# Performance work log

Hardware: AMD Instinct MI355X
Metric: run time of the kernel (lower is better)

The kernel has to match this reference:

```python
import jax, jax.numpy as jnp
import numpy as np
from jax import lax

NUM_TAGS = 64
PAD = 0


def setup_inputs() -> dict:
    key = jax.random.key(0)
    k1, k2, k3 = jax.random.split(key, 3)
    B, S, T = 128, 512, NUM_TAGS
    features = jax.random.normal(k1, (B, S, T), dtype=jnp.float32)
    labels = jax.random.randint(k2, (B, S), 0, T, dtype=jnp.int64)
    mask = jnp.ones((B, S), dtype=jnp.float32)
    transitions = jax.random.normal(k3, (T, T), dtype=jnp.float32)
    transitions = transitions.at[PAD, :].set(-10000.0)
    transitions = transitions.at[:, PAD].set(-10000.0)
    return {"features": features, "labels": labels, "mask": mask,
            "transitions": transitions}


def _score_sequence(emissions, labels, mask, transitions):
    # emission score at the gold labels, masked
    em = jnp.take_along_axis(emissions, labels[:, :, None], axis=2)[:, :, 0]
    seq_em = jnp.sum(em * mask, axis=1)
    # transition scores between consecutive gold labels
    tr = transitions[labels[:, :-1], labels[:, 1:]]
    tr_mask = mask[:, :-1] * mask[:, 1:]
    seq_tr = jnp.sum(tr * tr_mask, axis=1)
    return seq_em + seq_tr  # (B,)


def _log_partition(emissions, mask, transitions):
    # forward algorithm over the sequence via lax.scan
    alpha0 = emissions[:, 0, :]  # (B, T)
    em_rest = jnp.swapaxes(emissions[:, 1:, :], 0, 1)  # (S-1, B, T)
    mk_rest = jnp.swapaxes(mask[:, 1:], 0, 1)          # (S-1, B)

    def step(alpha, xs):
        em_t, m_t = xs
        # scores[b, i, j] = alpha[b, i] + transitions[i, j] + em_t[b, j]
        scores = alpha[:, :, None] + transitions[None, :, :] + em_t[:, None, :]
        new_alpha = jax.nn.logsumexp(scores, axis=1)  # (B, T)
        m = m_t[:, None]
        new_alpha = new_alpha * m + alpha * (1.0 - m)
        return new_alpha, None

    alpha, _ = lax.scan(step, alpha0, (em_rest, mk_rest))
    return jax.nn.logsumexp(alpha, axis=1)  # (B,)


def reference(features, labels, mask, transitions):
    gold = _score_sequence(features, labels, mask, transitions)
    logZ = _log_partition(features, mask, transitions)
    return jnp.mean(logZ - gold)  # scalar NLL
```

## Files before the change

### kernel.cpp

```cpp
#include <hip/hip_runtime.h>

#define B 128
#define S 512
#define T 64

typedef short bf16x8 __attribute__((ext_vector_type(8)));
typedef float f32x4 __attribute__((ext_vector_type(4)));
typedef _Float16 h2 __attribute__((ext_vector_type(2)));

__device__ __forceinline__ float rdlane(float v, int l) {
    return __int_as_float(__builtin_amdgcn_readlane(__float_as_int(v), l));
}
__device__ __forceinline__ unsigned cvtpk_bf16(float lo, float hi) {
    unsigned r;
    asm("v_cvt_pk_bf16_f32 %0, %1, %2" : "=v"(r) : "v"(lo), "v"(hi));
    return r;
}
__device__ __forceinline__ float fast_exp2(float x) {
    float r;
    asm("v_exp_f32 %0, %1" : "=v"(r) : "v"(x));
    return r;
}
__device__ __forceinline__ f32x4 mfma_init(bf16x8 a, bf16x8 b, f32x4 c0) {
    f32x4 d;
    asm volatile("v_mfma_f32_16x16x32_bf16 %0, %1, %2, %3"
                 : "=&v"(d) : "v"(a), "v"(b), "v"(c0));
    return d;
}
__device__ __forceinline__ void mfma_acc(f32x4& c, bf16x8 a, bf16x8 b) {
    asm volatile("v_mfma_f32_16x16x32_bf16 %0, %1, %2, %0"
                 : "+v"(c) : "v"(a), "v"(b));
}
__device__ __forceinline__ int krow(int kt, int gq, int e) {
    return 32 * kt + ((e >> 2) << 4) + 4 * gq + (e & 3);
}

template<int GG>
__global__ __launch_bounds__(256, 3)
void crf_chunk4(const float* __restrict__ features,
                const float* __restrict__ mask,
                const float* __restrict__ transitions,
                unsigned short* __restrict__ Zout,
                int* __restrict__ Kout)
{
    constexpr int CLT = S / GG;
    __shared__ unsigned short relay[4][T * 68];

    const int wid  = threadIdx.x >> 6;
    const int lane = threadIdx.x & 63;
    const int idx  = blockIdx.x * 4 + wid;
    const int b  = idx / GG;
    const int g  = idx % GG;
    const int c  = lane & 15;
    const int gq = lane >> 4;

    bf16x8 Ef[4][2];
    #pragma unroll
    for (int rt = 0; rt < 4; ++rt)
      #pragma unroll
      for (int kt = 0; kt < 2; ++kt) {
          unsigned dw[4];
          #pragma unroll
          for (int w = 0; w < 4; ++w) {
              int k0 = krow(kt, gq, 2 * w);
              float x0 = __expf(transitions[k0       * T + (c + 16*rt)]);
              float x1 = __expf(transitions[(k0 + 1) * T + (c + 16*rt)]);
              dw[w] = cvtpk_bf16(x0, x1);
          }
          uint4 q; q.x = dw[0]; q.y = dw[1]; q.z = dw[2]; q.w = dw[3];
          Ef[rt][kt] = __builtin_bit_cast(bf16x8, q);
      }

    bf16x8 Bf[2][4];
    #pragma unroll
    for (int kt = 0; kt < 2; ++kt)
      #pragma unroll
      for (int ct = 0; ct < 4; ++ct)
        #pragma unroll
        for (int e = 0; e < 8; ++e)
            Bf[kt][ct][e] = (krow(kt, gq, e) == 16*ct + c) ? (short)0x3F80
                                                           : (short)0;

    const float* fb = features + (size_t)b * S * T;
    const float* mb = mask + (size_t)b * S;
    const int t0 = g * CLT + 1;
    const int t1 = (g == GG - 1) ? S : (t0 + CLT);

    const f32x4 zero4 = {0.f, 0.f, 0.f, 0.f};

    int ktot = 0;
    float zloc = 1.0f;
    float mxr  = 1.0f;

    f32x4 emP[4];
    #pragma unroll
    for (int rt = 0; rt < 4; ++rt)
        emP[rt] = *(const f32x4*)(fb + t0 * T + 16*rt + 4*gq);
    float mP = mb[t0];

    for (int w = 0; w < CLT / 4; ++w) {
        #pragma unroll
        for (int j = 0; j < 4; ++j) {
            const int t = t0 + 4 * w + j;
            const bool act = (t < t1);

            f32x4 emc[4];
            #pragma unroll
            for (int rt = 0; rt < 4; ++rt) emc[rt] = emP[rt];
            float mc = mP;
            {
                int tn = min(t + 1, S - 1);
                #pragma unroll
                for (int rt = 0; rt < 4; ++rt)
                    emP[rt] = *(const f32x4*)(fb + tn * T + 16*rt + 4*gq);
                mP = mb[tn];
            }

            int kc = 0;
            if (j == 0) {
                kc = ((__float_as_int(mxr) >> 23) & 0xFF) - 127;
                kc = kc < -30 ? -30 : (kc > 60 ? 60 : kc);
            }

            if (act && mc != 0.0f) {
                if (j == 0) ktot += kc;
                const float kcf = (j == 0) ? (float)kc : 0.0f;

                f32x4 d4[4];
                #pragma unroll
                for (int rt = 0; rt < 4; ++rt)
                    #pragma unroll
                    for (int r = 0; r < 4; ++r)
                        d4[rt][r] = fast_exp2(fmaf(emc[rt][r], 1.44269504f, -kcf));

                #pragma unroll
                for (int ct = 0; ct < 4; ++ct) {
                    f32x4 Ct[4];
                    #pragma unroll
                    for (int tr = 0; tr < 4; ++tr) {
                        f32x4 z = mfma_init(Ef[tr][0], Bf[0][ct], zero4);
                        mfma_acc(z, Ef[tr][1], Bf[1][ct]);
                        Ct[tr] = z;
                    }
                    asm volatile("s_nop 7\ns_nop 7");
                    #pragma unroll
                    for (int tr = 0; tr < 4; ++tr) {
                        Ct[tr] *= d4[tr];
                        zloc = fmaxf(zloc, fmaxf(fmaxf(Ct[tr][0], Ct[tr][1]),
                                                 fmaxf(Ct[tr][2], Ct[tr][3])));
                    }
                    uint4 q0, q1;
                    q0.x = cvtpk_bf16(Ct[0][0], Ct[0][1]);
                    q0.y = cvtpk_bf16(Ct[0][2], Ct[0][3]);
                    q0.z = cvtpk_bf16(Ct[1][0], Ct[1][1]);
                    q0.w = cvtpk_bf16(Ct[1][2], Ct[1][3]);
                    q1.x = cvtpk_bf16(Ct[2][0], Ct[2][1]);
                    q1.y = cvtpk_bf16(Ct[2][2], Ct[2][3]);
                    q1.z = cvtpk_bf16(Ct[3][0], Ct[3][1]);
                    q1.w = cvtpk_bf16(Ct[3][2], Ct[3][3]);
                    Bf[0][ct] = __builtin_bit_cast(bf16x8, q0);
                    Bf[1][ct] = __builtin_bit_cast(bf16x8, q1);
                }
            }

            if (j == 2) {
                float mr = zloc;
                #pragma unroll
                for (int o = 32; o > 0; o >>= 1)
                    mr = fmaxf(mr, __shfl_xor(mr, o));
                mxr = mr; zloc = 1.0f;
            }
        }
    }

    unsigned short* rl = relay[wid];
    #pragma unroll
    for (int kt = 0; kt < 2; ++kt)
      #pragma unroll
      for (int ct = 0; ct < 4; ++ct) {
          uint4 q = __builtin_bit_cast(uint4, Bf[kt][ct]);
          int col = 16*ct + c;
          uint2 wa; wa.x = q.x; wa.y = q.y;
          uint2 wb; wb.x = q.z; wb.y = q.w;
          *(uint2*)&rl[col * 68 + 32*kt      + 4*gq] = wa;
          *(uint2*)&rl[col * 68 + 32*kt + 16 + 4*gq] = wb;
      }
    asm volatile("s_waitcnt lgkmcnt(0)" ::: "memory");

    unsigned short* zo = Zout + ((size_t)(b * GG + g)) * 64 * 64;
    #pragma unroll
    for (int q8 = 0; q8 < 8; ++q8) {
        unsigned dw[4];
        #pragma unroll
        for (int d = 0; d < 4; ++d) {
            unsigned lo = rl[(8*q8 + 2*d    ) * 68 + lane];
            unsigned hi = rl[(8*q8 + 2*d + 1) * 68 + lane];
            dw[d] = lo | (hi << 16);
        }
        uint4 wv; wv.x = dw[0]; wv.y = dw[1]; wv.z = dw[2]; wv.w = dw[3];
        *(uint4*)(zo + (size_t)lane * 64 + 8*q8) = wv;
    }
    if (lane == 0) Kout[b * GG + g] = ktot;
}

template<int GG>
__global__ __launch_bounds__(64, 1)
void crf_apply(const float* __restrict__ features,
               const int*   __restrict__ labels,
               const float* __restrict__ mask,
               const float* __restrict__ transitions,
               const unsigned short* __restrict__ Zmat,
               const int*   __restrict__ Kscale,
               float*       __restrict__ res)
{
    __shared__ float trans_lds[T * T];
    __shared__ float bcast[2][T];
    const int lane = threadIdx.x;
    const int b = blockIdx.x;

    for (int i = 0; i < T; ++i)
        trans_lds[i * T + lane] = transitions[i * T + lane];
    __syncthreads();

    const float* fb = features + (size_t)b * S * T;
    const int*   lb = labels + (size_t)b * S;
    const float* mb = mask + (size_t)b * S;

    float gold = 0.f;
    #pragma unroll
    for (int ch = 0; ch < S / T; ++ch) {
        int tt = ch * T + lane;
        int tm1 = tt > 0 ? tt - 1 : 0;
        int la = lb[tt], lp = lb[tm1];
        float mt = mb[tt], mp = mb[tm1];
        float em_g = fb[(size_t)tt * T + la];
        float tr_g = trans_lds[lp * T + la];
        gold += em_g * mt + ((tt > 0) ? tr_g * (mp * mt) : 0.f);
    }

    float a0 = fb[lane];
    float A0 = a0;
    #pragma unroll
    for (int o = 32; o > 0; o >>= 1) A0 = fmaxf(A0, __shfl_xor(A0, o));
    float v = __expf(a0 - A0);

    int esum = 0;

    const unsigned short* zb = Zmat + ((size_t)b * GG) * 64 * 64 + (size_t)lane * 64;
    uint4 cur[8], n1[8], n2[8];
    #pragma unroll
    for (int i = 0; i < 8; ++i) cur[i] = ((const uint4*)zb)[i];
    #pragma unroll
    for (int i = 0; i < 8; ++i) n1[i] = ((const uint4*)(zb + 64 * 64))[i];
    #pragma unroll
    for (int i = 0; i < 8; ++i) n2[i] = ((const uint4*)(zb + 2 * 64 * 64))[i];

    for (int g = 0; g < GG; ++g) {
        const int buf = g & 1;
        bcast[buf][lane] = v;
        asm volatile("s_waitcnt lgkmcnt(0)" ::: "memory");
        f32x4 vb[16];
        #pragma unroll
        for (int q = 0; q < 16; ++q) vb[q] = ((const f32x4*)bcast[buf])[q];

        float ac0 = 0.f, ac1 = 0.f, ac2 = 0.f, ac3 = 0.f;
        #pragma unroll
        for (int i = 0; i < 8; ++i) {
            unsigned zz[4] = {cur[i].x, cur[i].y, cur[i].z, cur[i].w};
            #pragma unroll
            for (int d = 0; d < 4; ++d) {
                int k = i * 8 + d * 2;
                float f0 = __int_as_float(zz[d] << 16);
                float f1 = __int_as_float(zz[d] & 0xFFFF0000u);
                if ((d & 1) == 0) { ac0 = fmaf(f0, vb[k >> 2][k & 3], ac0);
                                    ac1 = fmaf(f1, vb[(k+1) >> 2][(k+1) & 3], ac1); }
                else             { ac2 = fmaf(f0, vb[k >> 2][k & 3], ac2);
                                    ac3 = fmaf(f1, vb[(k+1) >> 2][(k+1) & 3], ac3); }
            }
        }
        float acc = (ac0 + ac1) + (ac2 + ac3);

        float a1 = fmaxf(rdlane(acc, 1), 1e-30f);
        int e = ((__float_as_int(a1) >> 23) & 0xFF) - 127;
        v = acc * __int_as_float((unsigned)(127 - e) << 23);
        esum += e + Kscale[b * GG + g];

        #pragma unroll
        for (int i = 0; i < 8; ++i) { cur[i] = n1[i]; n1[i] = n2[i]; }
        if (g + 3 < GG) {
            const uint4* zn = (const uint4*)(zb + (size_t)(g + 3) * 64 * 64);
            #pragma unroll
            for (int i = 0; i < 8; ++i) n2[i] = zn[i];
        }
    }

    float sum = v;
    #pragma unroll
    for (int o = 32; o > 0; o >>= 1) sum += __shfl_xor(sum, o);
    float logZ = __logf(fmaxf(sum, 1e-30f)) + A0 + (float)esum * 0.69314718056f;

    #pragma unroll
    for (int o = 32; o > 0; o >>= 1) gold += __shfl_xor(gold, o);

    if (lane == 0) res[b] = logZ - gold;
}

__global__ __launch_bounds__(64, 1)
void crf_fwd_seq(const float* __restrict__ features,
                 const int*   __restrict__ labels,
                 const float* __restrict__ mask,
                 const float* __restrict__ transitions,
                 float*       __restrict__ ws)
{
    __shared__ float trans_lds[T * T];
    __shared__ __align__(16) _Float16 ea_lds[2][T];

    const int lane = threadIdx.x;
    const int b    = blockIdx.x;

    for (int i = 0; i < T; ++i)
        trans_lds[i * T + lane] = transitions[i * T + lane];
    __syncthreads();

    h2 etr[T / 2];
    #pragma unroll
    for (int k = 0; k < T / 2; ++k) {
        etr[k].x = (_Float16)__expf(trans_lds[(2 * k + 0) * T + lane]);
        etr[k].y = (_Float16)__expf(trans_lds[(2 * k + 1) * T + lane]);
    }

    const float* fb = features + (size_t)b * S * T;
    const float* mb = mask + (size_t)b * S;
    const int*   lb = labels + (size_t)b * S;

    float alpha = fb[lane];
    float gold_part = 0.f;
    float M = 0.f;

    float em_n1 = fb[1 * T + lane];
    float em_n2 = fb[2 * T + lane];
    float em_n3 = fb[3 * T + lane];

    int   lab_c = lb[lane];
    int   lab_p = lb[lane > 0 ? lane - 1 : 0];
    float m_c   = mb[lane];
    float m_p   = mb[lane > 0 ? lane - 1 : 0];

    for (int ch = 0; ch < S / T; ++ch) {
        const int base = ch * T;
        const int tt   = base + lane;

        const int   glab  = lab_c;
        const int   glabp = lab_p;
        const float gmc   = m_c;
        const float gmp   = m_p;
        const float mreg  = m_c;

        float em_g = fb[(size_t)tt * T + glab];
        float tr_g = trans_lds[glabp * T + glab];

        {
            int tn  = tt + T;  if (tn > S - 1) tn = S - 1;
            int tnp = tn - 1;  if (tnp < 0) tnp = 0;
            lab_c = lb[tn]; lab_p = lb[tnp];
            m_c   = mb[tn]; m_p   = mb[tnp];
        }

        const int i0 = (ch == 0) ? 1 : 0;
        #pragma unroll 4
        for (int i = i0; i < T; ++i) {
            const int t = base + i;
            float em = em_n1;
            em_n1 = em_n2; em_n2 = em_n3;
            int tn = t + 3; if (tn > S - 1) tn = S - 1;
            em_n3 = fb[tn * T + lane];

            float ea = __expf(alpha - M);
            ea_lds[t & 1][lane] = (_Float16)ea;
            asm volatile("s_waitcnt lgkmcnt(0)" ::: "memory");

            const uint4* ep = (const uint4*)&ea_lds[t & 1][0];
            float a0 = 0.f, a1 = 0.f, a2 = 0.f, a3 = 0.f;
            #pragma unroll
            for (int q = 0; q < 8; ++q) {
                uint4 r = ep[q];
                a0 = __builtin_amdgcn_fdot2(__builtin_bit_cast(h2, r.x), etr[4 * q + 0], a0, false);
                a1 = __builtin_amdgcn_fdot2(__builtin_bit_cast(h2, r.y), etr[4 * q + 1], a1, false);
                a2 = __builtin_amdgcn_fdot2(__builtin_bit_cast(h2, r.z), etr[4 * q + 2], a2, false);
                a3 = __builtin_amdgcn_fdot2(__builtin_bit_cast(h2, r.w), etr[4 * q + 3], a3, false);
            }
            float s = (a0 + a1) + (a2 + a3);

            float m_t = rdlane(mreg, i);
            float s1  = rdlane(s, 1);
            float em1 = rdlane(em, 1);
            float Mn  = M + __logf(s1) + em1;

            float val = M + __logf(s) + em;
            val = fmaxf(val, -1e30f);
            alpha = val * m_t + alpha * (1.f - m_t);
            M     = (m_t > 0.5f) ? Mn : M;
        }

        float valid = (tt > 0) ? 1.f : 0.f;
        gold_part += em_g * gmc + tr_g * (gmp * gmc) * valid;
    }

    float M2 = alpha;
    #pragma unroll
    for (int o = 32; o > 0; o >>= 1) M2 = fmaxf(M2, __shfl_xor(M2, o));
    float e2 = __expf(alpha - M2);
    #pragma unroll
    for (int o = 32; o > 0; o >>= 1) e2 += __shfl_xor(e2, o);
    float logZ = M2 + __logf(e2);

    #pragma unroll
    for (int o = 32; o > 0; o >>= 1) gold_part += __shfl_xor(gold_part, o);

    if (lane == 0) ws[b] = logZ - gold_part;
}

__global__ __launch_bounds__(128)
void crf_reduce(const float* __restrict__ ws, float* __restrict__ out)
{
    const int tid = threadIdx.x;
    float v = ws[tid];
    #pragma unroll
    for (int o = 32; o > 0; o >>= 1) v += __shfl_xor(v, o);

    __shared__ float partial[2];
    if ((tid & 63) == 0) partial[tid >> 6] = v;
    __syncthreads();
    if (tid == 0) out[0] = (partial[0] + partial[1]) * (1.0f / (float)B);
}

extern "C" void kernel_launch(void* const* d_in, const int* in_sizes, int n_in,
                              void* d_out, int out_size, void* d_ws, size_t ws_size,
                              hipStream_t stream)
{
    const float* features    = (const float*)d_in[0];
    const int*   labels      = (const int*)  d_in[1];
    const float* mask        = (const float*)d_in[2];
    const float* transitions = (const float*)d_in[3];
    float* out = (float*)d_out;

    constexpr int GG = 16;
    const size_t zbytes = (size_t)B * GG * 64 * 64 * sizeof(unsigned short);
    const size_t kbytes = (size_t)B * GG * sizeof(int);
    const size_t need   = zbytes + kbytes + (size_t)B * sizeof(float);

    if (ws_size >= need) {
        unsigned short* Zmat = (unsigned short*)d_ws;
        int*   Ks  = (int*)((char*)d_ws + zbytes);
        float* res = (float*)((char*)d_ws + zbytes + kbytes);
        crf_chunk4<GG><<<dim3(B * GG / 4), dim3(256), 0, stream>>>(features, mask, transitions, Zmat, Ks);
        crf_apply<GG><<<dim3(B), dim3(64), 0, stream>>>(features, labels, mask, transitions, Zmat, Ks, res);
        crf_reduce<<<dim3(1), dim3(128), 0, stream>>>(res, out);
    } else {
        float* res = (float*)d_ws;
        crf_fwd_seq<<<dim3(B), dim3(64), 0, stream>>>(features, labels, mask, transitions, res);
        crf_reduce<<<dim3(1), dim3(128), 0, stream>>>(res, out);
    }
}
```

Before: 69.60 us.

## Split each chunk's 64 columns across four waves with per-column-group scales

The chunk kernel used to give one wave a whole 64x64 chunk product. It now uses one block per (batch, chunk), with each of the four waves carrying 16 columns. Each wave keeps its own exponent scale, so Kscale now stores four values per chunk, and the apply kernel rescales partial dot products by column group. This cuts the serial MFMA chain per step by four and quadruples the wave count, in exchange for more total exp/MFMA work (each wave still multiplies all 4 row tiles), a block-wide sync, and a shallower prefetch in the apply kernel.

```diff
diff --git a/kernel.cpp b/kernel.cpp
--- a/kernel.cpp
+++ b/kernel.cpp
@@ -21,38 +21,28 @@
     asm("v_exp_f32 %0, %1" : "=v"(r) : "v"(x));
     return r;
 }
-__device__ __forceinline__ f32x4 mfma_init(bf16x8 a, bf16x8 b, f32x4 c0) {
-    f32x4 d;
-    asm volatile("v_mfma_f32_16x16x32_bf16 %0, %1, %2, %3"
-                 : "=&v"(d) : "v"(a), "v"(b), "v"(c0));
-    return d;
-}
-__device__ __forceinline__ void mfma_acc(f32x4& c, bf16x8 a, bf16x8 b) {
-    asm volatile("v_mfma_f32_16x16x32_bf16 %0, %1, %2, %0"
-                 : "+v"(c) : "v"(a), "v"(b));
-}
 __device__ __forceinline__ int krow(int kt, int gq, int e) {
     return 32 * kt + ((e >> 2) << 4) + 4 * gq + (e & 3);
 }
 
 template<int GG>
-__global__ __launch_bounds__(256, 3)
-void crf_chunk4(const float* __restrict__ features,
-                const float* __restrict__ mask,
-                const float* __restrict__ transitions,
-                unsigned short* __restrict__ Zout,
-                int* __restrict__ Kout)
+__global__ __launch_bounds__(256, 4)
+void crf_col4(const float* __restrict__ features,
+              const float* __restrict__ mask,
+              const float* __restrict__ transitions,
+              unsigned short* __restrict__ Zout,
+              int* __restrict__ Kout)
 {
     constexpr int CLT = S / GG;
-    __shared__ unsigned short relay[4][T * 68];
+    __shared__ unsigned short relay[T * 68];
 
     const int wid  = threadIdx.x >> 6;
     const int lane = threadIdx.x & 63;
-    const int idx  = blockIdx.x * 4 + wid;
-    const int b  = idx / GG;
-    const int g  = idx % GG;
+    const int b  = blockIdx.x / GG;
+    const int g  = blockIdx.x % GG;
     const int c  = lane & 15;
     const int gq = lane >> 4;
+    const int mycol = 16 * wid + c;
 
     bf16x8 Ef[4][2];
     #pragma unroll
@@ -71,15 +61,12 @@
           Ef[rt][kt] = __builtin_bit_cast(bf16x8, q);
       }
 
-    bf16x8 Bf[2][4];
+    bf16x8 Bf[2];
     #pragma unroll
     for (int kt = 0; kt < 2; ++kt)
       #pragma unroll
-      for (int ct = 0; ct < 4; ++ct)
-        #pragma unroll
-        for (int e = 0; e < 8; ++e)
-            Bf[kt][ct][e] = (krow(kt, gq, e) == 16*ct + c) ? (short)0x3F80
-                                                           : (short)0;
+      for (int e = 0; e < 8; ++e)
+          Bf[kt][e] = (krow(kt, gq, e) == mycol) ? (short)0x3F80 : (short)0;
 
     const float* fb = features + (size_t)b * S * T;
     const float* mb = mask + (size_t)b * S;
@@ -89,8 +76,7 @@
     const f32x4 zero4 = {0.f, 0.f, 0.f, 0.f};
 
     int ktot = 0;
-    float zloc = 1.0f;
-    float mxr  = 1.0f;
+    float zloc = 1.0f, mxr = 1.0f;
 
     f32x4 emP[4];
     #pragma unroll
@@ -133,34 +119,28 @@
                     for (int r = 0; r < 4; ++r)
                         d4[rt][r] = fast_exp2(fmaf(emc[rt][r], 1.44269504f, -kcf));
 
+                f32x4 Ct[4];
                 #pragma unroll
-                for (int ct = 0; ct < 4; ++ct) {
-                    f32x4 Ct[4];
-                    #pragma unroll
-                    for (int tr = 0; tr < 4; ++tr) {
-                        f32x4 z = mfma_init(Ef[tr][0], Bf[0][ct], zero4);
-                        mfma_acc(z, Ef[tr][1], Bf[1][ct]);
-                        Ct[tr] = z;
-                    }
-                    asm volatile("s_nop 7\ns_nop 7");
-                    #pragma unroll
-                    for (int tr = 0; tr < 4; ++tr) {
-                        Ct[tr] *= d4[tr];
-                        zloc = fmaxf(zloc, fmaxf(fmaxf(Ct[tr][0], Ct[tr][1]),
-                                                 fmaxf(Ct[tr][2], Ct[tr][3])));
-                    }
-                    uint4 q0, q1;
-                    q0.x = cvtpk_bf16(Ct[0][0], Ct[0][1]);
-                    q0.y = cvtpk_bf16(Ct[0][2], Ct[0][3]);
-                    q0.z = cvtpk_bf16(Ct[1][0], Ct[1][1]);
-                    q0.w = cvtpk_bf16(Ct[1][2], Ct[1][3]);
-                    q1.x = cvtpk_bf16(Ct[2][0], Ct[2][1]);
-                    q1.y = cvtpk_bf16(Ct[2][2], Ct[2][3]);
-                    q1.z = cvtpk_bf16(Ct[3][0], Ct[3][1]);
-                    q1.w = cvtpk_bf16(Ct[3][2], Ct[3][3]);
-                    Bf[0][ct] = __builtin_bit_cast(bf16x8, q0);
-                    Bf[1][ct] = __builtin_bit_cast(bf16x8, q1);
+                for (int tr = 0; tr < 4; ++tr) {
+                    f32x4 z = __builtin_amdgcn_mfma_f32_16x16x32_bf16(Ef[tr][0], Bf[0], zero4, 0, 0, 0);
+                    z = __builtin_amdgcn_mfma_f32_16x16x32_bf16(Ef[tr][1], Bf[1], z, 0, 0, 0);
+                    Ct[tr] = z * d4[tr];
                 }
+                #pragma unroll
+                for (int tr = 0; tr < 4; ++tr)
+                    zloc = fmaxf(zloc, fmaxf(fmaxf(Ct[tr][0], Ct[tr][1]),
+                                             fmaxf(Ct[tr][2], Ct[tr][3])));
+                uint4 q0, q1;
+                q0.x = cvtpk_bf16(Ct[0][0], Ct[0][1]);
+                q0.y = cvtpk_bf16(Ct[0][2], Ct[0][3]);
+                q0.z = cvtpk_bf16(Ct[1][0], Ct[1][1]);
+                q0.w = cvtpk_bf16(Ct[1][2], Ct[1][3]);
+                q1.x = cvtpk_bf16(Ct[2][0], Ct[2][1]);
+                q1.y = cvtpk_bf16(Ct[2][2], Ct[2][3]);
+                q1.z = cvtpk_bf16(Ct[3][0], Ct[3][1]);
+                q1.w = cvtpk_bf16(Ct[3][2], Ct[3][3]);
+                Bf[0] = __builtin_bit_cast(bf16x8, q0);
+                Bf[1] = __builtin_bit_cast(bf16x8, q1);
             }
 
             if (j == 2) {
@@ -173,34 +153,36 @@
         }
     }
 
-    unsigned short* rl = relay[wid];
-    #pragma unroll
-    for (int kt = 0; kt < 2; ++kt)
-      #pragma unroll
-      for (int ct = 0; ct < 4; ++ct) {
-          uint4 q = __builtin_bit_cast(uint4, Bf[kt][ct]);
-          int col = 16*ct + c;
-          uint2 wa; wa.x = q.x; wa.y = q.y;
-          uint2 wb; wb.x = q.z; wb.y = q.w;
-          *(uint2*)&rl[col * 68 + 32*kt      + 4*gq] = wa;
-          *(uint2*)&rl[col * 68 + 32*kt + 16 + 4*gq] = wb;
-      }
-    asm volatile("s_waitcnt lgkmcnt(0)" ::: "memory");
-
-    unsigned short* zo = Zout + ((size_t)(b * GG + g)) * 64 * 64;
-    #pragma unroll
-    for (int q8 = 0; q8 < 8; ++q8) {
-        unsigned dw[4];
+    {
+        uint4 q = __builtin_bit_cast(uint4, Bf[0]);
+        uint4 p = __builtin_bit_cast(uint4, Bf[1]);
+        uint2 wa; wa.x = q.x; wa.y = q.y;
+        uint2 wb; wb.x = q.z; wb.y = q.w;
+        uint2 wc; wc.x = p.x; wc.y = p.y;
+        uint2 wd; wd.x = p.z; wd.y = p.w;
+        *(uint2*)&relay[mycol * 68 +      4*gq] = wa;
+        *(uint2*)&relay[mycol * 68 + 16 + 4*gq] = wb;
+        *(uint2*)&relay[mycol * 68 + 32 + 4*gq] = wc;
+        *(uint2*)&relay[mycol * 68 + 48 + 4*gq] = wd;
+    }
+    if (lane == 0) Kout[((size_t)b * GG + g) * 4 + wid] = ktot;
+    __syncthreads();
+
+    if (wid == 0) {
+        unsigned short* zo = Zout + ((size_t)(b * GG + g)) * 64 * 64;
         #pragma unroll
-        for (int d = 0; d < 4; ++d) {
-            unsigned lo = rl[(8*q8 + 2*d    ) * 68 + lane];
-            unsigned hi = rl[(8*q8 + 2*d + 1) * 68 + lane];
-            dw[d] = lo | (hi << 16);
-        }
-        uint4 wv; wv.x = dw[0]; wv.y = dw[1]; wv.z = dw[2]; wv.w = dw[3];
-        *(uint4*)(zo + (size_t)lane * 64 + 8*q8) = wv;
-    }
-    if (lane == 0) Kout[b * GG + g] = ktot;
+        for (int q8 = 0; q8 < 8; ++q8) {
+            unsigned dw[4];
+            #pragma unroll
+            for (int d = 0; d < 4; ++d) {
+                unsigned lo = relay[(8*q8 + 2*d    ) * 68 + lane];
+                unsigned hi = relay[(8*q8 + 2*d + 1) * 68 + lane];
+                dw[d] = lo | (hi << 16);
+            }
+            uint4 wv; wv.x = dw[0]; wv.y = dw[1]; wv.z = dw[2]; wv.w = dw[3];
+            *(uint4*)(zo + (size_t)lane * 64 + 8*q8) = wv;
+        }
+    }
 }
 
 template<int GG>
@@ -247,15 +229,18 @@
     int esum = 0;
 
     const unsigned short* zb = Zmat + ((size_t)b * GG) * 64 * 64 + (size_t)lane * 64;
-    uint4 cur[8], n1[8], n2[8];
+    uint4 cur[8], nxt[8];
     #pragma unroll
     for (int i = 0; i < 8; ++i) cur[i] = ((const uint4*)zb)[i];
-    #pragma unroll
-    for (int i = 0; i < 8; ++i) n1[i] = ((const uint4*)(zb + 64 * 64))[i];
-    #pragma unroll
-    for (int i = 0; i < 8; ++i) n2[i] = ((const uint4*)(zb + 2 * 64 * 64))[i];
 
     for (int g = 0; g < GG; ++g) {
+        if (g + 1 < GG) {
+            const uint4* zn = (const uint4*)(zb + (size_t)(g + 1) * 64 * 64);
+            #pragma unroll
+            for (int i = 0; i < 8; ++i) nxt[i] = zn[i];
+        }
+        int4 k4 = *(const int4*)(Kscale + ((size_t)b * GG + g) * 4);
+
         const int buf = g & 1;
         bcast[buf][lane] = v;
         asm volatile("s_waitcnt lgkmcnt(0)" ::: "memory");
@@ -263,35 +248,39 @@
         #pragma unroll
         for (int q = 0; q < 16; ++q) vb[q] = ((const f32x4*)bcast[buf])[q];
 
-        float ac0 = 0.f, ac1 = 0.f, ac2 = 0.f, ac3 = 0.f;
+        float s0 = 0.f, s1 = 0.f, s2 = 0.f, s3 = 0.f;
         #pragma unroll
         for (int i = 0; i < 8; ++i) {
             unsigned zz[4] = {cur[i].x, cur[i].y, cur[i].z, cur[i].w};
+            float part = 0.f;
             #pragma unroll
             for (int d = 0; d < 4; ++d) {
                 int k = i * 8 + d * 2;
                 float f0 = __int_as_float(zz[d] << 16);
                 float f1 = __int_as_float(zz[d] & 0xFFFF0000u);
-                if ((d & 1) == 0) { ac0 = fmaf(f0, vb[k >> 2][k & 3], ac0);
-                                    ac1 = fmaf(f1, vb[(k+1) >> 2][(k+1) & 3], ac1); }
-                else             { ac2 = fmaf(f0, vb[k >> 2][k & 3], ac2);
-                                    ac3 = fmaf(f1, vb[(k+1) >> 2][(k+1) & 3], ac3); }
-            }
-        }
-        float acc = (ac0 + ac1) + (ac2 + ac3);
+                part = fmaf(f0, vb[k >> 2][k & 3], part);
+                part = fmaf(f1, vb[(k + 1) >> 2][(k + 1) & 3], part);
+            }
+            if (i < 2)      s0 += part;
+            else if (i < 4) s1 += part;
+            else if (i < 6) s2 += part;
+            else            s3 += part;
+        }
+        int kmax = max(max(k4.x, k4.y), max(k4.z, k4.w));
+        int d0 = max(k4.x - kmax, -127), d1 = max(k4.y - kmax, -127);
+        int d2 = max(k4.z - kmax, -127), d3 = max(k4.w - kmax, -127);
+        float acc = s0 * __int_as_float((unsigned)(127 + d0) << 23)
+                  + s1 * __int_as_float((unsigned)(127 + d1) << 23)
+                  + s2 * __int_as_float((unsigned)(127 + d2) << 23)
+                  + s3 * __int_as_float((unsigned)(127 + d3) << 23);
 
         float a1 = fmaxf(rdlane(acc, 1), 1e-30f);
         int e = ((__float_as_int(a1) >> 23) & 0xFF) - 127;
         v = acc * __int_as_float((unsigned)(127 - e) << 23);
-        esum += e + Kscale[b * GG + g];
+        esum += e + kmax;
 
         #pragma unroll
-        for (int i = 0; i < 8; ++i) { cur[i] = n1[i]; n1[i] = n2[i]; }
-        if (g + 3 < GG) {
-            const uint4* zn = (const uint4*)(zb + (size_t)(g + 3) * 64 * 64);
-            #pragma unroll
-            for (int i = 0; i < 8; ++i) n2[i] = zn[i];
-        }
+        for (int i = 0; i < 8; ++i) cur[i] = nxt[i];
     }
 
     float sum = v;
@@ -446,14 +435,14 @@
 
     constexpr int GG = 16;
     const size_t zbytes = (size_t)B * GG * 64 * 64 * sizeof(unsigned short);
-    const size_t kbytes = (size_t)B * GG * sizeof(int);
+    const size_t kbytes = (size_t)B * GG * 4 * sizeof(int);
     const size_t need   = zbytes + kbytes + (size_t)B * sizeof(float);
 
     if (ws_size >= need) {
         unsigned short* Zmat = (unsigned short*)d_ws;
         int*   Ks  = (int*)((char*)d_ws + zbytes);
         float* res = (float*)((char*)d_ws + zbytes + kbytes);
-        crf_chunk4<GG><<<dim3(B * GG / 4), dim3(256), 0, stream>>>(features, mask, transitions, Zmat, Ks);
+        crf_col4<GG><<<dim3(B * GG), dim3(256), 0, stream>>>(features, mask, transitions, Zmat, Ks);
         crf_apply<GG><<<dim3(B), dim3(64), 0, stream>>>(features, labels, mask, transitions, Zmat, Ks, res);
         crf_reduce<<<dim3(1), dim3(128), 0, stream>>>(res, out);
     } else {
```

Measured after the change: 78.21 us. +12.4%, slower.
